# Performance work log

Hardware: AMD Instinct MI355X
Metric: run time of the kernel (lower is better)

The kernel has to match this reference:

```python
import jax, jax.numpy as jnp
import numpy as np

T, NE, NA, OBS, D, CH, VH, ITERS = 128, 64, 8, 64, 128, 128, 256, 2
B = NE * NA  # num_actors


def setup_inputs() -> dict:
    key = jax.random.key(0)
    ks = jax.random.split(key, 16)
    rn = lambda k, shape, s=0.05: jax.random.normal(k, shape, jnp.float32) * s
    z = lambda *shape: jnp.zeros(shape, jnp.float32)
    return dict(
        hidden=z(B, D),
        obs=rn(ks[0], (T, B, OBS), 1.0),
        dones=jax.random.bernoulli(ks[1], 0.05, (T, B)),
        embed1_w=rn(ks[2], (OBS, D)), embed1_b=z(D),
        embed2_w=rn(ks[3], (D, D)), embed2_b=z(D),
        gru_Wi=rn(ks[4], (D, 3 * D)), gru_bi=z(3 * D),
        gru_Wh=rn(ks[5], (D, 3 * D)), gru_bhn=z(D),
        couple_h_w=rn(ks[6], (2 * D, CH)), couple_h_b=z(CH),
        couple_out_w=rn(ks[7], (CH, 1)), couple_out_b=z(1),
        update_h_w=rn(ks[8], (2 * D, D)), update_h_b=z(D),
        update_out_w=rn(ks[9], (D, D)), update_out_b=z(D),
        value_h1_w=rn(ks[10], (D, VH)), value_h1_b=z(VH),
        value_h2_w=rn(ks[11], (VH, VH)), value_h2_b=z(VH),
        value_out_w=rn(ks[12], (VH, 1)), value_out_b=z(1),
    )


def _gru_scan(hidden, x, dones, Wi, bi, Wh, bhn):
    # flax GRUCell math: r,z gates (no hidden bias), n gate with hidden bias.
    def step(h, xd):
        xt, dt = xd
        h = jnp.where(dt[:, None], 0.0, h)  # reset carry on done
        gi = xt @ Wi + bi                   # [B, 3D]
        gh = h @ Wh                         # [B, 3D]
        i_r, i_z, i_n = jnp.split(gi, 3, axis=-1)
        h_r, h_z, h_n = jnp.split(gh, 3, axis=-1)
        r = jax.nn.sigmoid(i_r + h_r)
        zg = jax.nn.sigmoid(i_z + h_z)
        n = jnp.tanh(i_n + r * (h_n + bhn))
        new_h = (1.0 - zg) * n + zg * h
        return new_h, new_h
    return jax.lax.scan(step, hidden, (x, dones))


def reference(hidden, obs, dones,
              embed1_w, embed1_b, embed2_w, embed2_b,
              gru_Wi, gru_bi, gru_Wh, gru_bhn,
              couple_h_w, couple_h_b, couple_out_w, couple_out_b,
              update_h_w, update_h_b, update_out_w, update_out_b,
              value_h1_w, value_h1_b, value_h2_w, value_h2_b,
              value_out_w, value_out_b):
    # observation embedding MLP
    emb = jax.nn.relu(obs @ embed1_w + embed1_b)
    emb = jax.nn.relu(emb @ embed2_w + embed2_b)
    hidden, rnn_out = _gru_scan(hidden, emb, dones, gru_Wi, gru_bi, gru_Wh, gru_bhn)

    e = rnn_out.reshape(T, NE, NA, D)
    alive = (1.0 - dones.astype(jnp.float32)).reshape(T, NE, NA)
    e = e * alive[..., None]
    identity_mask = 1.0 - jnp.eye(NA, dtype=jnp.float32)

    # split-linear trick: couple_h(concat[h_i, h_j]) == h_i @ W1 + h_j @ W2 + b
    W1, W2 = couple_h_w[:D], couple_h_w[D:]
    U1, U2 = update_h_w[:D], update_h_w[D:]

    for _ in range(ITERS):
        a_i = jnp.einsum('teid,dh->teih', e, W1)  # [T,E,A,CH]
        a_j = jnp.einsum('tejd,dh->tejh', e, W2)
        Ch = jax.nn.relu(a_i[:, :, :, None, :] + a_j[:, :, None, :, :] + couple_h_b)  # [T,E,A,A,CH]
        C = jax.nn.sigmoid(jnp.einsum('teijh,h->teij', Ch, couple_out_w[:, 0]) + couple_out_b[0])
        C = C * alive[:, :, None, :] * identity_mask[None, None, :, :]
        context = jnp.einsum('teij,tejd->teid', C, e)
        delta = jax.nn.relu(e @ U1 + context @ U2 + update_h_b)
        delta = jax.nn.relu(delta @ update_out_w + update_out_b)
        e = (e + delta) * alive[..., None]

    v = jax.nn.relu(e @ value_h1_w + value_h1_b)
    v = jax.nn.relu(v @ value_h2_w + value_h2_b)
    v = (v @ value_out_w + value_out_b)[..., 0]  # [T,E,A]
    values = v.reshape(T, B)
    return hidden, values
```

## Files before the change

### kernel.cpp

```cpp
#include <hip/hip_runtime.h>
#include <hip/hip_bf16.h>
#include <math.h>

#define T_ 128
#define NE_ 64
#define NA_ 8
#define B_ 512
#define OBS_ 64
#define D_ 128
#define CH_ 128
#define VH_ 256
#define M_ (T_*B_)

typedef __attribute__((ext_vector_type(8))) short bf16x8;
typedef __attribute__((ext_vector_type(8))) _Float16 f16x8;
typedef __attribute__((ext_vector_type(4))) float f32x4;

__device__ __forceinline__ float sigmoidf_(float x){ return 1.f/(1.f+__expf(-x)); }
__device__ __forceinline__ unsigned short f2bu(float v){
  __hip_bfloat16 b = __float2bfloat16(v);
  return __builtin_bit_cast(unsigned short, b);
}
__device__ __forceinline__ float bu2f(unsigned short u){
  return __builtin_bit_cast(float, (unsigned int)u << 16);
}
__device__ __forceinline__ unsigned short f2hu(float v){
  _Float16 h = (_Float16)v;
  return __builtin_bit_cast(unsigned short, h);
}
__device__ __forceinline__ float hu2f(unsigned short u){
  return (float)__builtin_bit_cast(_Float16, u);
}

__global__ __launch_bounds__(512)
void embgi_k(const float* __restrict__ obs,
             const ushort* __restrict__ e1wT, const float* __restrict__ e1b,
             const ushort* __restrict__ e2wT, const float* __restrict__ e2b,
             const ushort* __restrict__ gWiT, const float* __restrict__ gbi,
             ushort* __restrict__ giH)
{
  __shared__ ushort S1[128*136];
  __shared__ ushort S2[128*136];
  const int tid  = threadIdx.x;
  const int lane = tid & 63, wave = tid >> 6;
  const int wm = wave >> 1, wn = wave & 1;
  const int quad = lane >> 4, ln = lane & 15;
  const int m0 = blockIdx.x * 128;

  f32x4 acc[2][4];

  #pragma unroll
  for (int i=0;i<4;i++){
    int c4 = tid + i*512;
    int m = c4 >> 4, kf = (c4 & 15) * 4;
    float4 v = *(const float4*)&obs[(size_t)(m0+m)*OBS_ + kf];
    ushort4 h; h.x=f2hu(v.x); h.y=f2hu(v.y); h.z=f2hu(v.z); h.w=f2hu(v.w);
    *(ushort4*)&S1[m*136 + kf] = h;
  }
  #pragma unroll
  for (int i=0;i<2;i++){
    int c8 = tid + i*512;
    int n = c8 >> 3, kq = (c8 & 7)*8;
    *(uint4*)&S2[n*136 + kq] = *(const uint4*)&e1wT[(size_t)n*64 + kq];
  }
  __syncthreads();

  #pragma unroll
  for (int i=0;i<2;i++)
    #pragma unroll
    for (int j=0;j<4;j++)
      #pragma unroll
      for (int r=0;r<4;r++) acc[i][j][r] = 0.f;
  #pragma unroll
  for (int ks=0; ks<2; ks++){
    const int kq = ks*32 + quad*8;
    f16x8 af[2], bfv[4];
    #pragma unroll
    for (int mt=0;mt<2;mt++)
      af[mt] = *(const f16x8*)&S1[(wm*32 + mt*16 + ln)*136 + kq];
    #pragma unroll
    for (int nt=0;nt<4;nt++)
      bfv[nt] = *(const f16x8*)&S2[(wn*64 + nt*16 + ln)*136 + kq];
    #pragma unroll
    for (int mt=0;mt<2;mt++)
      #pragma unroll
      for (int nt=0;nt<4;nt++)
        acc[mt][nt] = __builtin_amdgcn_mfma_f32_16x16x32_f16(af[mt], bfv[nt], acc[mt][nt], 0,0,0);
  }
  __syncthreads();

  #pragma unroll
  for (int mt=0;mt<2;mt++)
    #pragma unroll
    for (int r=0;r<4;r++){
      int rl = wm*32 + mt*16 + quad*4 + r;
      #pragma unroll
      for (int nt=0;nt<4;nt++){
        int cl = wn*64 + nt*16 + ln;
        S1[rl*136 + cl] = f2hu(fmaxf(acc[mt][nt][r] + e1b[cl], 0.f));
      }
    }
  #pragma unroll
  for (int i=0;i<4;i++){
    int c8 = tid + i*512;
    int n = c8 >> 4, kq = (c8 & 15)*8;
    *(uint4*)&S2[n*136 + kq] = *(const uint4*)&e2wT[(size_t)n*128 + kq];
  }
  __syncthreads();

  #pragma unroll
  for (int i=0;i<2;i++)
    #pragma unroll
    for (int j=0;j<4;j++)
      #pragma unroll
      for (int r=0;r<4;r++) acc[i][j][r] = 0.f;
  #pragma unroll
  for (int ks=0; ks<4; ks++){
    const int kq = ks*32 + quad*8;
    f16x8 af[2], bfv[4];
    #pragma unroll
    for (int mt=0;mt<2;mt++)
      af[mt] = *(const f16x8*)&S1[(wm*32 + mt*16 + ln)*136 + kq];
    #pragma unroll
    for (int nt=0;nt<4;nt++)
      bfv[nt] = *(const f16x8*)&S2[(wn*64 + nt*16 + ln)*136 + kq];
    #pragma unroll
    for (int mt=0;mt<2;mt++)
      #pragma unroll
      for (int nt=0;nt<4;nt++)
        acc[mt][nt] = __builtin_amdgcn_mfma_f32_16x16x32_f16(af[mt], bfv[nt], acc[mt][nt], 0,0,0);
  }
  __syncthreads();

  #pragma unroll
  for (int mt=0;mt<2;mt++)
    #pragma unroll
    for (int r=0;r<4;r++){
      int rl = wm*32 + mt*16 + quad*4 + r;
      #pragma unroll
      for (int nt=0;nt<4;nt++){
        int cl = wn*64 + nt*16 + ln;
        S1[rl*136 + cl] = f2hu(fmaxf(acc[mt][nt][r] + e2b[cl], 0.f));
      }
    }

  for (int c=0; c<3; c++){
    #pragma unroll
    for (int i=0;i<4;i++){
      int c8 = tid + i*512;
      int n = c8 >> 4, kq = (c8 & 15)*8;
      *(uint4*)&S2[n*136 + kq] = *(const uint4*)&gWiT[(size_t)(c*128+n)*128 + kq];
    }
    __syncthreads();
    #pragma unroll
    for (int i=0;i<2;i++)
      #pragma unroll
      for (int j=0;j<4;j++)
        #pragma unroll
        for (int r=0;r<4;r++) acc[i][j][r] = 0.f;
    #pragma unroll
    for (int ks=0; ks<4; ks++){
      const int kq = ks*32 + quad*8;
      f16x8 af[2], bfv[4];
      #pragma unroll
      for (int mt=0;mt<2;mt++)
        af[mt] = *(const f16x8*)&S1[(wm*32 + mt*16 + ln)*136 + kq];
      #pragma unroll
      for (int nt=0;nt<4;nt++)
        bfv[nt] = *(const f16x8*)&S2[(wn*64 + nt*16 + ln)*136 + kq];
      #pragma unroll
      for (int mt=0;mt<2;mt++)
        #pragma unroll
        for (int nt=0;nt<4;nt++)
          acc[mt][nt] = __builtin_amdgcn_mfma_f32_16x16x32_f16(af[mt], bfv[nt], acc[mt][nt], 0,0,0);
    }
    __syncthreads();
    #pragma unroll
    for (int mt=0;mt<2;mt++)
      #pragma unroll
      for (int r=0;r<4;r++){
        int row = m0 + wm*32 + mt*16 + quad*4 + r;
        #pragma unroll
        for (int nt=0;nt<4;nt++){
          int cl = wn*64 + nt*16 + ln;
          giH[(size_t)row*384 + c*128 + cl] = f2hu(acc[mt][nt][r] + gbi[c*128 + cl]);
        }
      }
  }
}

__global__ __launch_bounds__(512, 1)
void postgru_k(const __hip_bfloat16* __restrict__ Xe, const __hip_bfloat16* __restrict__ bcatT,
               const float* __restrict__ chb, const float* __restrict__ cow,
               const float* __restrict__ cob,
               const __hip_bfloat16* __restrict__ uhwT, const float* __restrict__ uhb,
               const __hip_bfloat16* __restrict__ uowT, const float* __restrict__ uob,
               const int* __restrict__ dones,
               const __hip_bfloat16* __restrict__ v1wT, const float* __restrict__ v1b,
               const __hip_bfloat16* __restrict__ v2wT, const float* __restrict__ v2b,
               const float* __restrict__ vow, const float* __restrict__ vob,
               float* __restrict__ values)
{
  __shared__ ushort S1[128*136];
  __shared__ ushort Bs[128*136];
  __shared__ alignas(16) ushort Pool[2*128*136];
  __shared__ alignas(16) float cbw[CH_], cww[CH_];
  __shared__ float Cs[4][NA_][NA_];
  __shared__ float SRed[128];
  const int tid  = threadIdx.x;
  const int lane = tid & 63, wave = tid >> 6;
  const int wm = wave >> 1, wn = wave & 1;
  const int quad = lane >> 4, ln = lane & 15;
  const int m0 = blockIdx.x * 128;

  ushort* XcS = Pool;
  float (*AI)[132] = (float(*)[132])(Pool + 128*136);
  float (*AJ)[132] = (float(*)[132])((char*)(Pool + 128*136) + 16896);

  #pragma unroll
  for (int i=0;i<4;i++){
    int c8 = tid + i*512;
    int m = c8 >> 4, kq = (c8 & 15)*8;
    *(uint4*)&S1[m*136 + kq] = *(const uint4*)((const ushort*)Xe + (size_t)(m0+m)*128 + kq);
  }
  if (tid < 128){ cbw[tid] = chb[tid]; cww[tid] = cow[tid]; }
  const float cob0 = cob[0];
  __syncthreads();

  for (int it=0; it<2; it++){
    for (int g=0; g<4; g++){
      const int r0 = g*32;
      const int wrow = wave >> 2;
      const int wcol = wave & 3;

      #pragma unroll
      for (int i=0;i<4;i++){
        int c8 = tid + i*512;
        int n = c8 >> 4, kq = (c8 & 15)*8;
        *(uint4*)&Bs[n*136 + kq] = *(const uint4*)((const ushort*)bcatT + (size_t)n*128 + kq);
      }
      __syncthreads();
      {
        f32x4 accc[2];
        #pragma unroll
        for (int nt=0;nt<2;nt++)
          #pragma unroll
          for (int r=0;r<4;r++) accc[nt][r] = 0.f;
        #pragma unroll
        for (int ks=0; ks<4; ks++){
          const int kq = ks*32 + quad*8;
          bf16x8 af = *(const bf16x8*)&S1[(r0 + wrow*16 + ln)*136 + kq];
          #pragma unroll
          for (int nt=0;nt<2;nt++){
            bf16x8 bfv = *(const bf16x8*)&Bs[(wcol*32 + nt*16 + ln)*136 + kq];
            accc[nt] = __builtin_amdgcn_mfma_f32_16x16x32_bf16(af, bfv, accc[nt], 0,0,0);
          }
        }
        __syncthreads();
        #pragma unroll
        for (int nt=0;nt<2;nt++)
          #pragma unroll
          for (int r=0;r<4;r++)
            AI[wrow*16 + quad*4 + r][wcol*32 + nt*16 + ln] = accc[nt][r];
      }
      #pragma unroll
      for (int i=0;i<4;i++){
        int c8 = tid + i*512;
        int n = c8 >> 4, kq = (c8 & 15)*8;
        *(uint4*)&Bs[n*136 + kq] = *(const uint4*)((const ushort*)bcatT + (size_t)(128+n)*128 + kq);
      }
      __syncthreads();
      {
        f32x4 accc[2];
        #pragma unroll
        for (int nt=0;nt<2;nt++)
          #pragma unroll
          for (int r=0;r<4;r++) accc[nt][r] = 0.f;
        #pragma unroll
        for (int ks=0; ks<4; ks++){
          const int kq = ks*32 + quad*8;
          bf16x8 af = *(const bf16x8*)&S1[(r0 + wrow*16 + ln)*136 + kq];
          #pragma unroll
          for (int nt=0;nt<2;nt++){
            bf16x8 bfv = *(const bf16x8*)&Bs[(wcol*32 + nt*16 + ln)*136 + kq];
            accc[nt] = __builtin_amdgcn_mfma_f32_16x16x32_bf16(af, bfv, accc[nt], 0,0,0);
          }
        }
        #pragma unroll
        for (int nt=0;nt<2;nt++)
          #pragma unroll
          for (int r=0;r<4;r++)
            AJ[wrow*16 + quad*4 + r][wcol*32 + nt*16 + ln] = accc[nt][r];
      }
      __syncthreads();

      {
        const int env = tid >> 7;
        const int i   = (tid >> 4) & 7;
        const int jg  = (tid >> 3) & 1;
        const int hq  = tid & 7;
        const float* aiR = &AI[env*8 + i][0];
        const float* aj0 = &AJ[env*8 + jg*4 + 0][0];
        const float* aj1 = &AJ[env*8 + jg*4 + 1][0];
        const float* aj2 = &AJ[env*8 + jg*4 + 2][0];
        const float* aj3 = &AJ[env*8 + jg*4 + 3][0];
        float s0=0.f, s1=0.f, s2=0.f, s3=0.f;
        #pragma unroll
        for (int t=0; t<4; t++){
          int h = (hq + t*8)*4;
          float4 a4 = *(const float4*)&aiR[h];
          float4 c4 = *(const float4*)&cbw[h];
          float4 w4 = *(const float4*)&cww[h];
          float px = a4.x + c4.x, py = a4.y + c4.y, pz = a4.z + c4.z, pw = a4.w + c4.w;
          float4 b0 = *(const float4*)&aj0[h];
          s0 += fmaxf(px+b0.x,0.f)*w4.x + fmaxf(py+b0.y,0.f)*w4.y
              + fmaxf(pz+b0.z,0.f)*w4.z + fmaxf(pw+b0.w,0.f)*w4.w;
          float4 b1 = *(const float4*)&aj1[h];
          s1 += fmaxf(px+b1.x,0.f)*w4.x + fmaxf(py+b1.y,0.f)*w4.y
              + fmaxf(pz+b1.z,0.f)*w4.z + fmaxf(pw+b1.w,0.f)*w4.w;
          float4 b2 = *(const float4*)&aj2[h];
          s2 += fmaxf(px+b2.x,0.f)*w4.x + fmaxf(py+b2.y,0.f)*w4.y
              + fmaxf(pz+b2.z,0.f)*w4.z + fmaxf(pw+b2.w,0.f)*w4.w;
          float4 b3 = *(const float4*)&aj3[h];
          s3 += fmaxf(px+b3.x,0.f)*w4.x + fmaxf(py+b3.y,0.f)*w4.y
              + fmaxf(pz+b3.z,0.f)*w4.z + fmaxf(pw+b3.w,0.f)*w4.w;
        }
        s0 += __shfl_xor(s0,1); s0 += __shfl_xor(s0,2); s0 += __shfl_xor(s0,4);
        s1 += __shfl_xor(s1,1); s1 += __shfl_xor(s1,2); s1 += __shfl_xor(s1,4);
        s2 += __shfl_xor(s2,1); s2 += __shfl_xor(s2,2); s2 += __shfl_xor(s2,4);
        s3 += __shfl_xor(s3,1); s3 += __shfl_xor(s3,2); s3 += __shfl_xor(s3,4);
        if (hq == 0){
          int j0 = jg*4;
          float c0 = sigmoidf_(s0 + cob0); Cs[env][i][j0+0] = (i==j0+0)?0.f:c0;
          float c1 = sigmoidf_(s1 + cob0); Cs[env][i][j0+1] = (i==j0+1)?0.f:c1;
          float c2 = sigmoidf_(s2 + cob0); Cs[env][i][j0+2] = (i==j0+2)?0.f:c2;
          float c3 = sigmoidf_(s3 + cob0); Cs[env][i][j0+3] = (i==j0+3)?0.f:c3;
        }
      }
      __syncthreads();

      {
        const int lr = tid >> 4;
        const int env = lr >> 3, ii = lr & 7;
        const int c0 = (tid & 15) * 8;
        #pragma unroll
        for (int cc=0; cc<2; cc++){
          int d = c0 + cc*4;
          float a0=0.f, a1=0.f, a2=0.f, a3=0.f;
          #pragma unroll
          for (int j=0;j<NA_;j++){
            float c = Cs[env][ii][j];
            ushort4 e4 = *(const ushort4*)&S1[(r0 + env*8 + j)*136 + d];
            a0 = fmaf(c, bu2f(e4.x), a0);
            a1 = fmaf(c, bu2f(e4.y), a1);
            a2 = fmaf(c, bu2f(e4.z), a2);
            a3 = fmaf(c, bu2f(e4.w), a3);
          }
          ushort4 o; o.x=f2bu(a0); o.y=f2bu(a1); o.z=f2bu(a2); o.w=f2bu(a3);
          *(ushort4*)&XcS[(r0 + lr)*136 + d] = o;
        }
      }
      __syncthreads();
    }

    f32x4 acc[2][4];
    #pragma unroll
    for (int i=0;i<2;i++)
      #pragma unroll
      for (int j=0;j<4;j++)
        #pragma unroll
        for (int r=0;r<4;r++) acc[i][j][r] = 0.f;

    #pragma unroll
    for (int kc=0; kc<2; kc++){
      #pragma unroll
      for (int i=0;i<4;i++){
        int c8 = tid + i*512;
        int n = c8 >> 4, kq = (c8 & 15)*8;
        *(uint4*)&Bs[n*136 + kq] = *(const uint4*)((const ushort*)uhwT + (size_t)n*256 + kc*128 + kq);
      }
      __syncthreads();
      const ushort* Ab = kc ? XcS : S1;
      #pragma unroll
      for (int ks=0; ks<4; ks++){
        const int kq = ks*32 + quad*8;
        bf16x8 af[2], bfv[4];
        #pragma unroll
        for (int mt=0;mt<2;mt++)
          af[mt] = *(const bf16x8*)&Ab[(wm*32 + mt*16 + ln)*136 + kq];
        #pragma unroll
        for (int nt=0;nt<4;nt++)
          bfv[nt] = *(const bf16x8*)&Bs[(wn*64 + nt*16 + ln)*136 + kq];
        #pragma unroll
        for (int mt=0;mt<2;mt++)
          #pragma unroll
          for (int nt=0;nt<4;nt++)
            acc[mt][nt] = __builtin_amdgcn_mfma_f32_16x16x32_bf16(af[mt], bfv[nt], acc[mt][nt], 0,0,0);
      }
      __syncthreads();
    }

    #pragma unroll
    for (int i=0;i<4;i++){
      int c8 = tid + i*512;
      int n = c8 >> 4, kq = (c8 & 15)*8;
      *(uint4*)&Bs[n*136 + kq] = *(const uint4*)((const ushort*)uowT + (size_t)n*128 + kq);
    }
    #pragma unroll
    for (int mt=0;mt<2;mt++)
      #pragma unroll
      for (int r=0;r<4;r++){
        int rl = wm*32 + mt*16 + quad*4 + r;
        #pragma unroll
        for (int nt=0;nt<4;nt++){
          int cl = wn*64 + nt*16 + ln;
          XcS[rl*136 + cl] = f2bu(fmaxf(acc[mt][nt][r] + uhb[cl], 0.f));
        }
      }
    __syncthreads();

    f32x4 acc2[2][4];
    #pragma unroll
    for (int i=0;i<2;i++)
      #pragma unroll
      for (int j=0;j<4;j++)
        #pragma unroll
        for (int r=0;r<4;r++) acc2[i][j][r] = 0.f;
    #pragma unroll
    for (int ks=0; ks<4; ks++){
      const int kq = ks*32 + quad*8;
      bf16x8 af[2], bfv[4];
      #pragma unroll
      for (int mt=0;mt<2;mt++)
        af[mt] = *(const bf16x8*)&XcS[(wm*32 + mt*16 + ln)*136 + kq];
      #pragma unroll
      for (int nt=0;nt<4;nt++)
        bfv[nt] = *(const bf16x8*)&Bs[(wn*64 + nt*16 + ln)*136 + kq];
      #pragma unroll
      for (int mt=0;mt<2;mt++)
        #pragma unroll
        for (int nt=0;nt<4;nt++)
          acc2[mt][nt] = __builtin_amdgcn_mfma_f32_16x16x32_bf16(af[mt], bfv[nt], acc2[mt][nt], 0,0,0);
    }
    #pragma unroll
    for (int mt=0;mt<2;mt++){
      #pragma unroll
      for (int r=0;r<4;r++){
        int rl = wm*32 + mt*16 + quad*4 + r;
        int row = m0 + rl;
        float al = (dones[row]!=0) ? 0.f : 1.f;
        #pragma unroll
        for (int nt=0;nt<4;nt++){
          int cl = wn*64 + nt*16 + ln;
          float v = fmaxf(acc2[mt][nt][r] + uob[cl], 0.f);
          v += bu2f(S1[rl*136 + cl]);
          v *= al;
          S1[rl*136 + cl] = f2bu(v);
        }
      }
    }
    __syncthreads();
  }

  ushort* V1 = Pool;

  for (int h=0; h<2; h++){
    #pragma unroll
    for (int i=0;i<4;i++){
      int c8 = tid + i*512;
      int n = c8 >> 4, kq = (c8 & 15)*8;
      *(uint4*)&Bs[n*136 + kq] = *(const uint4*)((const ushort*)v1wT + (size_t)(h*128+n)*128 + kq);
    }
    __syncthreads();
    f32x4 acc[2][4];
    #pragma unroll
    for (int i=0;i<2;i++)
      #pragma unroll
      for (int j=0;j<4;j++)
        #pragma unroll
        for (int r=0;r<4;r++) acc[i][j][r] = 0.f;
    #pragma unroll
    for (int ks=0; ks<4; ks++){
      const int kq = ks*32 + quad*8;
      bf16x8 af[2], bfv[4];
      #pragma unroll
      for (int mt=0;mt<2;mt++)
        af[mt] = *(const bf16x8*)&S1[(wm*32 + mt*16 + ln)*136 + kq];
      #pragma unroll
      for (int nt=0;nt<4;nt++)
        bfv[nt] = *(const bf16x8*)&Bs[(wn*64 + nt*16 + ln)*136 + kq];
      #pragma unroll
      for (int mt=0;mt<2;mt++)
        #pragma unroll
        for (int nt=0;nt<4;nt++)
          acc[mt][nt] = __builtin_amdgcn_mfma_f32_16x16x32_bf16(af[mt], bfv[nt], acc[mt][nt], 0,0,0);
    }
    __syncthreads();
    #pragma unroll
    for (int mt=0;mt<2;mt++)
      #pragma unroll
      for (int r=0;r<4;r++){
        int rl = wm*32 + mt*16 + quad*4 + r;
        #pragma unroll
        for (int nt=0;nt<4;nt++){
          int cl = wn*64 + nt*16 + ln;
          V1[h*128*136 + rl*136 + cl] = f2bu(fmaxf(acc[mt][nt][r] + v1b[h*128 + cl], 0.f));
        }
      }
  }

  float s[2][4];
  #pragma unroll
  for (int mt=0;mt<2;mt++)
    #pragma unroll
    for (int r=0;r<4;r++) s[mt][r] = 0.f;

  for (int oc=0; oc<2; oc++){
    f32x4 acc[2][4];
    #pragma unroll
    for (int i=0;i<2;i++)
      #pragma unroll
      for (int j=0;j<4;j++)
        #pragma unroll
        for (int r=0;r<4;r++) acc[i][j][r] = 0.f;
    for (int kh=0; kh<2; kh++){
      #pragma unroll
      for (int i=0;i<4;i++){
        int c8 = tid + i*512;
        int n = c8 >> 4, kq = (c8 & 15)*8;
        *(uint4*)&Bs[n*136 + kq] = *(const uint4*)((const ushort*)v2wT + (size_t)(oc*128+n)*256 + kh*128 + kq);
      }
      __syncthreads();
      #pragma unroll
      for (int ks=0; ks<4; ks++){
        const int kq = ks*32 + quad*8;
        bf16x8 af[2], bfv[4];
        #pragma unroll
        for (int mt=0;mt<2;mt++)
          af[mt] = *(const bf16x8*)&V1[kh*128*136 + (wm*32 + mt*16 + ln)*136 + kq];
        #pragma unroll
        for (int nt=0;nt<4;nt++)
          bfv[nt] = *(const bf16x8*)&Bs[(wn*64 + nt*16 + ln)*136 + kq];
        #pragma unroll
        for (int mt=0;mt<2;mt++)
          #pragma unroll
          for (int nt=0;nt<4;nt++)
            acc[mt][nt] = __builtin_amdgcn_mfma_f32_16x16x32_bf16(af[mt], bfv[nt], acc[mt][nt], 0,0,0);
      }
      __syncthreads();
    }
    float v2bv[4], voww[4];
    #pragma unroll
    for (int nt=0;nt<4;nt++){
      int col = oc*128 + wn*64 + nt*16 + ln;
      v2bv[nt] = v2b[col];
      voww[nt] = vow[col];
    }
    #pragma unroll
    for (int mt=0;mt<2;mt++)
      #pragma unroll
      for (int r=0;r<4;r++){
        float p = 0.f;
        #pragma unroll
        for (int nt=0;nt<4;nt++)
          p += fmaxf(acc[mt][nt][r] + v2bv[nt], 0.f) * voww[nt];
        s[mt][r] += p;
      }
  }

  #pragma unroll
  for (int off=1; off<16; off<<=1)
    #pragma unroll
    for (int mt=0;mt<2;mt++)
      #pragma unroll
      for (int r=0;r<4;r++)
        s[mt][r] += __shfl_xor(s[mt][r], off);
  if (ln == 0 && wn == 1){
    #pragma unroll
    for (int mt=0;mt<2;mt++)
      #pragma unroll
      for (int r=0;r<4;r++)
        SRed[wm*32 + mt*16 + quad*4 + r] = s[mt][r];
  }
  __syncthreads();
  if (ln == 0 && wn == 0){
    float vob0 = vob[0];
    #pragma unroll
    for (int mt=0;mt<2;mt++)
      #pragma unroll
      for (int r=0;r<4;r++){
        int rl = wm*32 + mt*16 + quad*4 + r;
        values[m0 + rl] = s[mt][r] + SRed[rl] + vob0;
      }
  }
}

__global__ __launch_bounds__(512, 1)
void grum8_k(const ushort* __restrict__ gih, const float* __restrict__ hidden0,
             const int* __restrict__ dones, const float* __restrict__ gWh,
             const float* __restrict__ bhn, __hip_bfloat16* __restrict__ eb_out,
             float* __restrict__ hout)
{
  __shared__ ushort wstg[32*392];
  __shared__ ushort hb[2][16*136];
  __shared__ float  dnS[T_*4];
  const int tid  = threadIdx.x;
  const int lane = tid & 63, wave = tid >> 6;
  const int quad = lane >> 4, ln = lane & 15;
  const int r0   = blockIdx.x * 4;
  const int col  = wave*16 + ln;
  const int lnb  = ln & 12;

  dnS[tid] = (dones[(size_t)(tid>>2)*B_ + r0 + (tid&3)] != 0) ? 1.f : 0.f;
  const float bhnr = bhn[col];

  for (int i=tid; i<16*136; i+=512){ hb[0][i]=0; hb[1][i]=0; }

  f16x8 bf[3][4];
  #pragma unroll
  for (int kc=0; kc<4; kc++){
    for (int i=tid; i<32*384; i+=512){
      int kk = i/384, c = i - kk*384;
      wstg[kk*392 + c] = f2hu(gWh[(size_t)(kc*32+kk)*384 + c]);
    }
    __syncthreads();
    #pragma unroll
    for (int g=0; g<3; g++){
      int c = g*128 + col;
      ushort tmp[8];
      #pragma unroll
      for (int j=0;j<8;j++) tmp[j] = wstg[(quad*8+j)*392 + c];
      bf[g][kc] = *(const f16x8*)tmp;
    }
    __syncthreads();
  }

  float hc = hidden0[(size_t)(r0+quad)*D_ + col];
  if (dnS[quad] > 0.5f) hc = 0.f;
  hb[0][(quad*4)*136 + col] = f2hu(hc);
  __syncthreads();

  const ushort* gbase = gih + ((size_t)(r0+quad))*384;
  const size_t  gstep = (size_t)B_*384;

  float c_r, c_z, c_n;
  c_r = hu2f(gbase[col]); c_z = hu2f(gbase[col+128]); c_n = hu2f(gbase[col+256]);
  ushort aR,aZ,aN, bR,bZ,bN, cR,cZ,cN, dR,dZ,dN;
  { const ushort* gp = gbase + 1*gstep; aR = gp[col]; aZ = gp[col+128]; aN = gp[col+256]; }
  { const ushort* gp = gbase + 2*gstep; bR = gp[col]; bZ = gp[col+128]; bN = gp[col+256]; }
  { const ushort* gp = gbase + 3*gstep; cR = gp[col]; cZ = gp[col+128]; cN = gp[col+256]; }
  dR=0; dZ=0; dN=0;

  ushort pend_eu = 0;

#define GSTEP(t, IR,IZ,IN, OR,OZ,ON)                                          \
  {                                                                           \
    if ((t) > 0)                                                              \
      ((ushort*)eb_out)[((size_t)((t)-1)*B_ + r0+quad)*D_ + col] = pend_eu;   \
    { int tl = (t)+4; if (tl > T_-1) tl = T_-1;                               \
      const ushort* gp = gbase + (size_t)tl*gstep;                            \
      OR = gp[col]; OZ = gp[col+128]; ON = gp[col+256]; }                     \
    const ushort* hbuf = hb[(t)&1];                                           \
    f32x4 accA[3], accB[3];                                                   \
    _Pragma("unroll")                                                         \
    for (int g=0;g<3;g++){                                                    \
      _Pragma("unroll")                                                       \
      for (int r=0;r<4;r++){ accA[g][r]=0.f; accB[g][r]=0.f; }                \
    }                                                                         \
    _Pragma("unroll")                                                         \
    for (int ks=0; ks<2; ks++){                                               \
      f16x8 ahA = *(const f16x8*)&hbuf[lnb*136 + (2*ks  )*32 + quad*8];       \
      f16x8 ahB = *(const f16x8*)&hbuf[lnb*136 + (2*ks+1)*32 + quad*8];       \
      _Pragma("unroll")                                                       \
      for (int g=0;g<3;g++){                                                  \
        accA[g] = __builtin_amdgcn_mfma_f32_16x16x32_f16(ahA, bf[g][2*ks  ], accA[g], 0,0,0); \
        accB[g] = __builtin_amdgcn_mfma_f32_16x16x32_f16(ahB, bf[g][2*ks+1], accB[g], 0,0,0); \
      }                                                                       \
    }                                                                         \
    const float dnow  = dnS[(t)*4 + quad];                                    \
    const float dnext = ((t)+1 < T_) ? dnS[((t)+1)*4 + quad] : 0.f;           \
    float rg = sigmoidf_(c_r + accA[0][0] + accB[0][0]);                      \
    float zg = sigmoidf_(c_z + accA[1][0] + accB[1][0]);                      \
    float x  = c_n + rg*(accA[2][0] + accB[2][0] + bhnr);                     \
    float ng = 2.f/(1.f+__expf(-2.f*x)) - 1.f;                                \
    float hnew = (1.f - zg)*ng + zg*hc;                                       \
    pend_eu = f2bu(hnew*(1.f-dnow));                                          \
    float hv = (dnext > 0.5f) ? 0.f : hnew;                                   \
    hc = hv;                                                                  \
    hb[((t)+1)&1][(quad*4)*136 + col] = f2hu(hv);                             \
    asm volatile("s_waitcnt lgkmcnt(0)\n\ts_barrier" ::: "memory");           \
    c_r = hu2f(IR); c_z = hu2f(IZ); c_n = hu2f(IN);                           \
  }

  for (int t=0; t<T_; t+=4){
    GSTEP(t+0, aR,aZ,aN, dR,dZ,dN);
    GSTEP(t+1, bR,bZ,bN, aR,aZ,aN);
    GSTEP(t+2, cR,cZ,cN, bR,bZ,bN);
    GSTEP(t+3, dR,dZ,dN, cR,cZ,cN);
  }
#undef GSTEP

  ((ushort*)eb_out)[((size_t)(T_-1)*B_ + r0+quad)*D_ + col] = pend_eu;
  hout[(size_t)(r0+quad)*D_ + col] = hc;
}

__global__ __launch_bounds__(256)
void packall_k(const float* __restrict__ e1w, ushort* __restrict__ e1T,
               const float* __restrict__ e2w, ushort* __restrict__ e2T,
               const float* __restrict__ gWi, ushort* __restrict__ giT,
               const float* __restrict__ chw, __hip_bfloat16* __restrict__ bcatT,
               const float* __restrict__ uhw, __hip_bfloat16* __restrict__ uhwT,
               const float* __restrict__ uow, __hip_bfloat16* __restrict__ uowT,
               const float* __restrict__ v1w, __hip_bfloat16* __restrict__ v1wT,
               const float* __restrict__ v2w, __hip_bfloat16* __restrict__ v2wT)
{
  const int b = blockIdx.x, tid = threadIdx.x;
  if (b < 32){
    int idx = b*256 + tid;
    int n = idx >> 6, k = idx & 63;
    e1T[idx] = f2hu(e1w[k*128 + n]);
  } else if (b < 96){
    int idx = (b-32)*256 + tid;
    int n = idx >> 7, k = idx & 127;
    e2T[idx] = f2hu(e2w[k*128 + n]);
  } else if (b < 288){
    int idx = (b-96)*256 + tid;
    int n = idx >> 7, k = idx & 127;
    giT[idx] = f2hu(gWi[k*384 + n]);
  } else if (b < 416){
    int idx = (b-288)*256 + tid;
    int n = idx >> 7, k = idx & 127;
    float v = (n < 128) ? chw[k*128 + n] : chw[(128+k)*128 + (n-128)];
    bcatT[idx] = __float2bfloat16(v);
  } else if (b < 544){
    int idx = (b-416)*256 + tid;
    int r = idx >> 7, c = idx & 127;
    uhwT[c*256 + r] = __float2bfloat16(uhw[idx]);
  } else if (b < 608){
    int idx = (b-544)*256 + tid;
    int r = idx >> 7, c = idx & 127;
    uowT[c*128 + r] = __float2bfloat16(uow[idx]);
  } else if (b < 736){
    int idx = (b-608)*256 + tid;
    int r = idx >> 8, c = idx & 255;
    v1wT[c*128 + r] = __float2bfloat16(v1w[idx]);
  } else {
    int idx = (b-736)*256 + tid;
    int r = idx >> 8, c = idx & 255;
    v2wT[c*256 + r] = __float2bfloat16(v2w[idx]);
  }
}

extern "C" void kernel_launch(void* const* d_in, const int* in_sizes, int n_in,
                              void* d_out, int out_size, void* d_ws, size_t ws_size,
                              hipStream_t stream) {
  const float* hidden = (const float*)d_in[0];
  const float* obs    = (const float*)d_in[1];
  const int*   dones  = (const int*)  d_in[2];
  const float* e1w = (const float*)d_in[3];
  const float* e1b = (const float*)d_in[4];
  const float* e2w = (const float*)d_in[5];
  const float* e2b = (const float*)d_in[6];
  const float* gWi = (const float*)d_in[7];
  const float* gbi = (const float*)d_in[8];
  const float* gWh = (const float*)d_in[9];
  const float* gbhn= (const float*)d_in[10];
  const float* chw = (const float*)d_in[11];
  const float* chb = (const float*)d_in[12];
  const float* cow = (const float*)d_in[13];
  const float* cob = (const float*)d_in[14];
  const float* uhw = (const float*)d_in[15];
  const float* uhb = (const float*)d_in[16];
  const float* uow = (const float*)d_in[17];
  const float* uob = (const float*)d_in[18];
  const float* v1w = (const float*)d_in[19];
  const float* v1b = (const float*)d_in[20];
  const float* v2w = (const float*)d_in[21];
  const float* v2b = (const float*)d_in[22];
  const float* vow = (const float*)d_in[23];
  const float* vob = (const float*)d_in[24];
  (void)in_sizes; (void)n_in; (void)out_size;

  float* out_hidden = (float*)d_out;
  float* out_values = (float*)d_out + (size_t)B_*D_;

  float* ws = (float*)d_ws;
  ushort* giH   = (ushort*)(ws + 10485760);
  __hip_bfloat16* Xe = (__hip_bfloat16*)(ws + 23068672);
  ushort* wb    = (ushort*)(ws + 27262976);
  if (ws_size < (size_t)27500000 * sizeof(float)) return;

  __hip_bfloat16* bcatT = (__hip_bfloat16*)wb;
  __hip_bfloat16* uhwT  = (__hip_bfloat16*)wb + 32768;
  __hip_bfloat16* uowT  = (__hip_bfloat16*)wb + 65536;
  __hip_bfloat16* v1wT  = (__hip_bfloat16*)wb + 81920;
  __hip_bfloat16* v2wT  = (__hip_bfloat16*)wb + 114688;
  ushort* e1wT = wb + 180224;
  ushort* e2wT = wb + 188416;
  ushort* gWiT = wb + 204800;

  dim3 blk(256);
  packall_k<<<dim3(992), blk, 0, stream>>>(
    e1w, e1wT, e2w, e2wT, gWi, gWiT,
    chw, bcatT, uhw, uhwT, uow, uowT, v1w, v1wT, v2w, v2wT);

  embgi_k<<<dim3(512), dim3(512), 0, stream>>>(obs, e1wT, e1b, e2wT, e2b, gWiT, gbi, giH);

  grum8_k<<<dim3(128), dim3(512), 0, stream>>>(giH, hidden, dones, gWh, gbhn, Xe, out_hidden);

  postgru_k<<<dim3(512), dim3(512), 0, stream>>>(Xe, bcatT, chb, cow, cob,
                                                 uhwT, uhb, uowT, uob, dones,
                                                 v1wT, v1b, v2wT, v2b, vow, vob, out_values);
}
```

Baseline: 309.5 us.

## Read MFMA weight fragments directly from global memory instead of LDS staging

```diff
diff --git a/kernel.cpp b/kernel.cpp
--- a/kernel.cpp
+++ b/kernel.cpp
@@ -202,7 +202,6 @@
                float* __restrict__ values)
 {
   __shared__ ushort S1[128*136];
-  __shared__ ushort Bs[128*136];
   __shared__ alignas(16) ushort Pool[2*128*136];
   __shared__ alignas(16) float cbw[CH_], cww[CH_];
   __shared__ float Cs[4][NA_][NA_];
@@ -213,6 +212,12 @@
   const int quad = lane >> 4, ln = lane & 15;
   const int m0 = blockIdx.x * 128;
 
+  const ushort* bcat = (const ushort*)bcatT;
+  const ushort* uhw  = (const ushort*)uhwT;
+  const ushort* uow  = (const ushort*)uowT;
+  const ushort* v1w  = (const ushort*)v1wT;
+  const ushort* v2w  = (const ushort*)v2wT;
+
   ushort* XcS = Pool;
   float (*AI)[132] = (float(*)[132])(Pool + 128*136);
   float (*AJ)[132] = (float(*)[132])((char*)(Pool + 128*136) + 16896);
@@ -233,64 +238,32 @@
       const int wrow = wave >> 2;
       const int wcol = wave & 3;
 
-      #pragma unroll
-      for (int i=0;i<4;i++){
-        int c8 = tid + i*512;
-        int n = c8 >> 4, kq = (c8 & 15)*8;
-        *(uint4*)&Bs[n*136 + kq] = *(const uint4*)((const ushort*)bcatT + (size_t)n*128 + kq);
-      }
-      __syncthreads();
       {
-        f32x4 accc[2];
+        f32x4 accI[2], accJ[2];
         #pragma unroll
         for (int nt=0;nt<2;nt++)
           #pragma unroll
-          for (int r=0;r<4;r++) accc[nt][r] = 0.f;
+          for (int r=0;r<4;r++){ accI[nt][r] = 0.f; accJ[nt][r] = 0.f; }
         #pragma unroll
         for (int ks=0; ks<4; ks++){
           const int kq = ks*32 + quad*8;
           bf16x8 af = *(const bf16x8*)&S1[(r0 + wrow*16 + ln)*136 + kq];
           #pragma unroll
           for (int nt=0;nt<2;nt++){
-            bf16x8 bfv = *(const bf16x8*)&Bs[(wcol*32 + nt*16 + ln)*136 + kq];
-            accc[nt] = __builtin_amdgcn_mfma_f32_16x16x32_bf16(af, bfv, accc[nt], 0,0,0);
+            int n = wcol*32 + nt*16 + ln;
+            bf16x8 b1 = *(const bf16x8*)&bcat[(size_t)n*128 + kq];
+            bf16x8 b2 = *(const bf16x8*)&bcat[(size_t)(128+n)*128 + kq];
+            accI[nt] = __builtin_amdgcn_mfma_f32_16x16x32_bf16(af, b1, accI[nt], 0,0,0);
+            accJ[nt] = __builtin_amdgcn_mfma_f32_16x16x32_bf16(af, b2, accJ[nt], 0,0,0);
           }
         }
-        __syncthreads();
         #pragma unroll
         for (int nt=0;nt<2;nt++)
           #pragma unroll
-          for (int r=0;r<4;r++)
-            AI[wrow*16 + quad*4 + r][wcol*32 + nt*16 + ln] = accc[nt][r];
-      }
-      #pragma unroll
-      for (int i=0;i<4;i++){
-        int c8 = tid + i*512;
-        int n = c8 >> 4, kq = (c8 & 15)*8;
-        *(uint4*)&Bs[n*136 + kq] = *(const uint4*)((const ushort*)bcatT + (size_t)(128+n)*128 + kq);
-      }
-      __syncthreads();
-      {
-        f32x4 accc[2];
-        #pragma unroll
-        for (int nt=0;nt<2;nt++)
-          #pragma unroll
-          for (int r=0;r<4;r++) accc[nt][r] = 0.f;
-        #pragma unroll
-        for (int ks=0; ks<4; ks++){
-          const int kq = ks*32 + quad*8;
-          bf16x8 af = *(const bf16x8*)&S1[(r0 + wrow*16 + ln)*136 + kq];
-          #pragma unroll
-          for (int nt=0;nt<2;nt++){
-            bf16x8 bfv = *(const bf16x8*)&Bs[(wcol*32 + nt*16 + ln)*136 + kq];
-            accc[nt] = __builtin_amdgcn_mfma_f32_16x16x32_bf16(af, bfv, accc[nt], 0,0,0);
+          for (int r=0;r<4;r++){
+            AI[wrow*16 + quad*4 + r][wcol*32 + nt*16 + ln] = accI[nt][r];
+            AJ[wrow*16 + quad*4 + r][wcol*32 + nt*16 + ln] = accJ[nt][r];
           }
-        }
-        #pragma unroll
-        for (int nt=0;nt<2;nt++)
-          #pragma unroll
-          for (int r=0;r<4;r++)
-            AJ[wrow*16 + quad*4 + r][wcol*32 + nt*16 + ln] = accc[nt][r];
       }
       __syncthreads();
 
@@ -373,13 +346,6 @@
 
     #pragma unroll
     for (int kc=0; kc<2; kc++){
-      #pragma unroll
-      for (int i=0;i<4;i++){
-        int c8 = tid + i*512;
-        int n = c8 >> 4, kq = (c8 & 15)*8;
-        *(uint4*)&Bs[n*136 + kq] = *(const uint4*)((const ushort*)uhwT + (size_t)n*256 + kc*128 + kq);
-      }
-      __syncthreads();
       const ushort* Ab = kc ? XcS : S1;
       #pragma unroll
       for (int ks=0; ks<4; ks++){
@@ -389,23 +355,19 @@
         for (int mt=0;mt<2;mt++)
           af[mt] = *(const bf16x8*)&Ab[(wm*32 + mt*16 + ln)*136 + kq];
         #pragma unroll
-        for (int nt=0;nt<4;nt++)
-          bfv[nt] = *(const bf16x8*)&Bs[(wn*64 + nt*16 + ln)*136 + kq];
+        for (int nt=0;nt<4;nt++){
+          int n = wn*64 + nt*16 + ln;
+          bfv[nt] = *(const bf16x8*)&uhw[(size_t)n*256 + kc*128 + kq];
+        }
         #pragma unroll
         for (int mt=0;mt<2;mt++)
           #pragma unroll
           for (int nt=0;nt<4;nt++)
             acc[mt][nt] = __builtin_amdgcn_mfma_f32_16x16x32_bf16(af[mt], bfv[nt], acc[mt][nt], 0,0,0);
       }
-      __syncthreads();
-    }
-
-    #pragma unroll
-    for (int i=0;i<4;i++){
-      int c8 = tid + i*512;
-      int n = c8 >> 4, kq = (c8 & 15)*8;
-      *(uint4*)&Bs[n*136 + kq] = *(const uint4*)((const ushort*)uowT + (size_t)n*128 + kq);
-    }
+    }
+    __syncthreads();
+
     #pragma unroll
     for (int mt=0;mt<2;mt++)
       #pragma unroll
@@ -434,8 +396,10 @@
       for (int mt=0;mt<2;mt++)
         af[mt] = *(const bf16x8*)&XcS[(wm*32 + mt*16 + ln)*136 + kq];
       #pragma unroll
-      for (int nt=0;nt<4;nt++)
-        bfv[nt] = *(const bf16x8*)&Bs[(wn*64 + nt*16 + ln)*136 + kq];
+      for (int nt=0;nt<4;nt++){
+        int n = wn*64 + nt*16 + ln;
+        bfv[nt] = *(const bf16x8*)&uow[(size_t)n*128 + kq];
+      }
       #pragma unroll
       for (int mt=0;mt<2;mt++)
         #pragma unroll
@@ -464,14 +428,8 @@
 
   ushort* V1 = Pool;
 
+  #pragma unroll
   for (int h=0; h<2; h++){
-    #pragma unroll
-    for (int i=0;i<4;i++){
-      int c8 = tid + i*512;
-      int n = c8 >> 4, kq = (c8 & 15)*8;
-      *(uint4*)&Bs[n*136 + kq] = *(const uint4*)((const ushort*)v1wT + (size_t)(h*128+n)*128 + kq);
-    }
-    __syncthreads();
     f32x4 acc[2][4];
     #pragma unroll
     for (int i=0;i<2;i++)
@@ -487,15 +445,16 @@
       for (int mt=0;mt<2;mt++)
         af[mt] = *(const bf16x8*)&S1[(wm*32 + mt*16 + ln)*136 + kq];
       #pragma unroll
-      for (int nt=0;nt<4;nt++)
-        bfv[nt] = *(const bf16x8*)&Bs[(wn*64 + nt*16 + ln)*136 + kq];
+      for (int nt=0;nt<4;nt++){
+        int n = wn*64 + nt*16 + ln;
+        bfv[nt] = *(const bf16x8*)&v1w[(size_t)(h*128+n)*128 + kq];
+      }
       #pragma unroll
       for (int mt=0;mt<2;mt++)
         #pragma unroll
         for (int nt=0;nt<4;nt++)
           acc[mt][nt] = __builtin_amdgcn_mfma_f32_16x16x32_bf16(af[mt], bfv[nt], acc[mt][nt], 0,0,0);
     }
-    __syncthreads();
     #pragma unroll
     for (int mt=0;mt<2;mt++)
       #pragma unroll
@@ -508,6 +467,7 @@
         }
       }
   }
+  __syncthreads();
 
   float s[2][4];
   #pragma unroll
@@ -523,14 +483,8 @@
       for (int j=0;j<4;j++)
         #pragma unroll
         for (int r=0;r<4;r++) acc[i][j][r] = 0.f;
+    #pragma unroll
     for (int kh=0; kh<2; kh++){
-      #pragma unroll
-      for (int i=0;i<4;i++){
-        int c8 = tid + i*512;
-        int n = c8 >> 4, kq = (c8 & 15)*8;
-        *(uint4*)&Bs[n*136 + kq] = *(const uint4*)((const ushort*)v2wT + (size_t)(oc*128+n)*256 + kh*128 + kq);
-      }
-      __syncthreads();
       #pragma unroll
       for (int ks=0; ks<4; ks++){
         const int kq = ks*32 + quad*8;
@@ -539,15 +493,16 @@
         for (int mt=0;mt<2;mt++)
           af[mt] = *(const bf16x8*)&V1[kh*128*136 + (wm*32 + mt*16 + ln)*136 + kq];
         #pragma unroll
-        for (int nt=0;nt<4;nt++)
-          bfv[nt] = *(const bf16x8*)&Bs[(wn*64 + nt*16 + ln)*136 + kq];
+        for (int nt=0;nt<4;nt++){
+          int n = wn*64 + nt*16 + ln;
+          bfv[nt] = *(const bf16x8*)&v2w[(size_t)(oc*128+n)*256 + kh*128 + kq];
+        }
         #pragma unroll
         for (int mt=0;mt<2;mt++)
           #pragma unroll
           for (int nt=0;nt<4;nt++)
             acc[mt][nt] = __builtin_amdgcn_mfma_f32_16x16x32_bf16(af[mt], bfv[nt], acc[mt][nt], 0,0,0);
       }
-      __syncthreads();
     }
     float v2bv[4], voww[4];
     #pragma unroll
```

Result: slower. 374.9 us (+21.2%).
